# Performance work log

Measured on AMD Instinct MI355X. Metric: run time of the kernel, lower is better.

The kernel has to match this reference:

```python
import jax, jax.numpy as jnp
import numpy as np
from jax import lax


def _layernorm(x, g, b, eps=1e-5):
    m = x.mean(-1, keepdims=True)
    v = ((x - m) ** 2).mean(-1, keepdims=True)
    return (x - m) * lax.rsqrt(v + eps) * g + b


def _conv1d(x, w, b):
    # x: (B, T, Cin), w: (K, Cin, Cout) -> SAME padding (kernel=3, pad=1)
    y = lax.conv_general_dilated(x, w, (1,), 'SAME',
                                 dimension_numbers=('NWC', 'WIO', 'NWC'))
    return y + b


def _predictor(x, params, mask):
    w1, b1, g1, be1, w2, b2, g2, be2, wl, bl = params
    h = _layernorm(jax.nn.relu(_conv1d(x, w1, b1)), g1, be1)
    h = _layernorm(jax.nn.relu(_conv1d(h, w2, b2)), g2, be2)
    out = (h @ wl)[..., 0] + bl[0]          # (B, T)
    return jnp.where(mask, 0.0, out)


def _length_regulate(x, dur, max_len):
    # vectorized equivalent of the per-token expand/cat/pad loop
    cum = jnp.cumsum(dur, axis=1)            # (B, S)
    mel_len = cum[:, -1]                     # (B,)
    pos = jnp.arange(max_len)                # (T,)
    idx = jax.vmap(lambda c: jnp.searchsorted(c, pos, side='right'))(cum)
    idx = jnp.minimum(idx, x.shape[1] - 1)   # (B, T)
    out = jnp.take_along_axis(x, idx[:, :, None], axis=1)
    valid = (pos[None, :] < mel_len[:, None])[:, :, None]
    return jnp.where(valid, out, 0.0), mel_len


def setup_inputs() -> dict:
    key = jax.random.key(0)
    ks = jax.random.split(key, 12)
    B, S, D, F, K, T, NB = 32, 512, 512, 512, 3, 4096, 256
    inp = {
        'x': jax.random.normal(ks[0], (B, S, D), jnp.float32),
        'src_mask': jnp.zeros((B, S), bool),
        'mel_mask': jnp.zeros((B, T), bool),
        'pitch_truth': jax.random.normal(ks[1], (B, S), jnp.float32),
        'energy_truth': jax.random.normal(ks[2], (B, S), jnp.float32),
        'duration_truth': jax.random.randint(ks[3], (B, S), 0, 8, jnp.int32),
        'conv1_w': 0.05 * jax.random.normal(ks[4], (3, K, D, F), jnp.float32),
        'conv1_b': jnp.zeros((3, F), jnp.float32),
        'ln1_g': jnp.ones((3, F), jnp.float32),
        'ln1_b': jnp.zeros((3, F), jnp.float32),
        'conv2_w': 0.05 * jax.random.normal(ks[5], (3, K, F, F), jnp.float32),
        'conv2_b': jnp.zeros((3, F), jnp.float32),
        'ln2_g': jnp.ones((3, F), jnp.float32),
        'ln2_b': jnp.zeros((3, F), jnp.float32),
        'lin_w': 0.05 * jax.random.normal(ks[6], (3, F, 1), jnp.float32),
        'lin_b': jnp.zeros((3, 1), jnp.float32),
        'pitch_emb': 0.05 * jax.random.normal(ks[7], (NB, D), jnp.float32),
        'energy_emb': 0.05 * jax.random.normal(ks[8], (NB, D), jnp.float32),
        'pitch_bins': jnp.linspace(-3.0, 3.0, NB - 1),
        'energy_bins': jnp.linspace(-3.0, 3.0, NB - 1),
        'max_mel_len': T,
    }
    return inp


def reference(x, src_mask, mel_mask, pitch_truth, energy_truth, duration_truth,
              conv1_w, conv1_b, ln1_g, ln1_b, conv2_w, conv2_b, ln2_g, ln2_b,
              lin_w, lin_b, pitch_emb, energy_emb, pitch_bins, energy_bins,
              max_mel_len):
    def params(i):
        return (conv1_w[i], conv1_b[i], ln1_g[i], ln1_b[i],
                conv2_w[i], conv2_b[i], ln2_g[i], ln2_b[i], lin_w[i], lin_b[i])

    # pitch (predictor idx 0)
    pitch_pred = _predictor(x, params(0), src_mask)
    x = x + pitch_emb[jnp.searchsorted(pitch_bins, pitch_truth, side='left')]
    # energy (idx 1)
    energy_pred = _predictor(x, params(1), src_mask)
    x = x + energy_emb[jnp.searchsorted(energy_bins, energy_truth, side='left')]
    # duration (idx 2)
    log_dur = _predictor(x, params(2), src_mask)
    # length regulation with ground-truth durations (training path)
    x_out, mel_len = _length_regulate(x, duration_truth, max_mel_len)
    return x_out, pitch_pred, energy_pred, log_dur, mel_len, mel_mask
```

## Files before the change

kernel.cpp:

```cpp
#include <hip/hip_runtime.h>
#include <hip/hip_bf16.h>


#define B_ 32
#define S_ 512
#define D_ 512
#define F_ 512
#define T_ 4096
#define SP_ 514
#define KK_ 1536
#define NKT 24

typedef __attribute__((ext_vector_type(8))) short bf16x8;
typedef __attribute__((ext_vector_type(4))) float f32x4;

__device__ __forceinline__ float bf2f(unsigned short u) {
  union { unsigned int i; float f; } c; c.i = (unsigned int)u << 16; return c.f;
}
__device__ __forceinline__ unsigned short f2bf(float f) {
  __hip_bfloat16 h = __float2bfloat16(f);
  return *(unsigned short*)&h;
}

#define WT_BLKS 1152
#define TP_BLKS 8224
__global__ __launch_bounds__(256) void prep_k(const float* __restrict__ x,
                                              const float* __restrict__ W1,
                                              const float* __restrict__ W2,
                                              const int* __restrict__ dur,
                                              __hip_bfloat16* __restrict__ X0,
                                              __hip_bfloat16* __restrict__ X,
                                              __hip_bfloat16* __restrict__ P,
                                              __hip_bfloat16* __restrict__ WT1,
                                              __hip_bfloat16* __restrict__ WT2,
                                              int* __restrict__ cum,
                                              float* __restrict__ mel_len) {
  const int blk = blockIdx.x;
  const int t = threadIdx.x;
  if (blk < WT_BLKS) {
    __shared__ float tb[64][65];
    const int w = blk / 192;
    const int kt = (blk % 192) >> 3;
    const int ft = blk & 7;
    const float* src = (w < 3) ? (W1 + (size_t)w * KK_ * F_)
                               : (W2 + (size_t)(w - 3) * KK_ * F_);
    __hip_bfloat16* dst = (w < 3) ? (WT1 + (size_t)w * KK_ * F_)
                                  : (WT2 + (size_t)(w - 3) * KK_ * F_);
    const int ty = t >> 4, tx = t & 15;
    #pragma unroll
    for (int j = 0; j < 4; ++j) {
      const int r = ty + j * 16;
      const float4 v = *(const float4*)(src + (size_t)(kt * 64 + r) * F_ + ft * 64 + tx * 4);
      tb[r][tx * 4 + 0] = v.x; tb[r][tx * 4 + 1] = v.y;
      tb[r][tx * 4 + 2] = v.z; tb[r][tx * 4 + 3] = v.w;
    }
    __syncthreads();
    #pragma unroll
    for (int j = 0; j < 4; ++j) {
      const int r = ty + j * 16;
      ushort4 u = make_ushort4(f2bf(tb[tx * 4 + 0][r]), f2bf(tb[tx * 4 + 1][r]),
                               f2bf(tb[tx * 4 + 2][r]), f2bf(tb[tx * 4 + 3][r]));
      *(ushort4*)((unsigned short*)dst + (size_t)(ft * 64 + r) * KK_ + kt * 64 + tx * 4) = u;
    }
  } else if (blk < WT_BLKS + TP_BLKS) {
    const int task = (blk - WT_BLKS) * 2 + (t >> 7);
    const int tl = t & 127;
    if (task < B_ * S_) {
      const int b = task >> 9, s = task & 511;
      const float4 v = *(const float4*)(x + (size_t)task * D_ + tl * 4);
      ushort4 u = make_ushort4(f2bf(v.x), f2bf(v.y), f2bf(v.z), f2bf(v.w));
      *(ushort4*)((unsigned short*)X0 + ((size_t)b * SP_ + s + 1) * D_ + tl * 4) = u;
    } else {
      const int idx = task - B_ * S_;
      const int b = idx >> 1;
      const int r = (idx & 1) ? (SP_ - 1) : 0;
      const size_t off = ((size_t)b * SP_ + r) * D_ + tl * 4;
      const ushort4 z = make_ushort4(0, 0, 0, 0);
      *(ushort4*)((unsigned short*)X0 + off) = z;
      *(ushort4*)((unsigned short*)X + off) = z;
      *(ushort4*)((unsigned short*)P + off) = z;
    }
  } else {
    __shared__ int sh[S_];
    const int b = blk - (WT_BLKS + TP_BLKS);
    sh[t] = dur[b * S_ + t];
    sh[t + 256] = dur[b * S_ + t + 256];
    __syncthreads();
    for (int off = 1; off < S_; off <<= 1) {
      const int a1 = (t >= off) ? sh[t - off] : 0;
      const int j2 = t + 256;
      const int a2 = (j2 >= off) ? sh[j2 - off] : 0;
      __syncthreads();
      sh[t] += a1; sh[j2] += a2;
      __syncthreads();
    }
    cum[b * S_ + t] = sh[t];
    cum[b * S_ + t + 256] = sh[t + 256];
    if (t == 255) mel_len[b] = (float)sh[S_ - 1];
  }
}

template <int MODE>
__global__ __launch_bounds__(512, 1) void convfuse_k(
    const __hip_bfloat16* __restrict__ Pin,
    const __hip_bfloat16* __restrict__ WT,
    const float* __restrict__ bias,
    const float* __restrict__ g,
    const float* __restrict__ be,
    const float* __restrict__ wl,
    const float* __restrict__ bl,
    const unsigned char* __restrict__ mask,
    __hip_bfloat16* __restrict__ Pout,
    float* __restrict__ pred,
    const float* __restrict__ truth,
    const float* __restrict__ bins,
    const float* __restrict__ embp,
    const __hip_bfloat16* __restrict__ Xsrc,
    __hip_bfloat16* __restrict__ Xdst) {
  extern __shared__ char smem[];
  char* As = smem;
  char* Bs = smem + 2 * 8192;
  const int swz = (blockIdx.x & 7) * 32 + (blockIdx.x >> 3);
  const int b  = swz >> 3;
  const int st = (swz & 7) * 64;
  const int t = threadIdx.x;
  const int lane = t & 63;
  const int wave = t >> 6;
  const int wn = wave * 64;

  f32x4 acc[4][4];
  #pragma unroll
  for (int m = 0; m < 4; ++m)
    #pragma unroll
    for (int n = 0; n < 4; ++n) acc[m][n] = (f32x4){0.f, 0.f, 0.f, 0.f};

  const __hip_bfloat16* Xb = Pin + (size_t)b * SP_ * D_;

  auto stage = [&](int kt, int buf) {
    const int tap = kt >> 3, d0 = (kt & 7) * 64;
    const __hip_bfloat16* Arow = Xb + (size_t)(st + tap) * D_ + d0;
    char* Ad = As + buf * 8192;
    {
      const int row = t >> 3, ch = t & 7;
      const __hip_bfloat16* ga = Arow + (size_t)row * D_ + (ch ^ (row & 7)) * 8;
      __builtin_amdgcn_global_load_lds(
          (const __attribute__((address_space(1))) void*)ga,
          (__attribute__((address_space(3))) void*)(Ad + t * 16), 16, 0, 0);
    }
    char* Bd = Bs + buf * 65536;
    #pragma unroll
    for (int i = 0; i < 8; ++i) {
      const int c = t + i * 512;
      const int fr = c >> 3, ch = c & 7;
      const __hip_bfloat16* gb = WT + (size_t)fr * KK_ + kt * 64 + (ch ^ (fr & 7)) * 8;
      __builtin_amdgcn_global_load_lds(
          (const __attribute__((address_space(1))) void*)gb,
          (__attribute__((address_space(3))) void*)(Bd + c * 16), 16, 0, 0);
    }
  };

  stage(0, 0);
  const int rA = lane & 15;
  const int kc16 = (lane >> 4) * 16;
  const int sw = (rA & 7) << 4;

  for (int kt = 0; kt < NKT; ++kt) {
    const int cur = kt & 1;
    if (kt < NKT - 1) {
      stage(kt + 1, cur ^ 1);
      asm volatile("s_waitcnt vmcnt(9)" ::: "memory");
    } else {
      asm volatile("s_waitcnt vmcnt(0)" ::: "memory");
    }
    __builtin_amdgcn_s_barrier();
    __builtin_amdgcn_sched_barrier(0);
    const char* Ab = As + cur * 8192;
    const char* Bb = Bs + cur * 65536;
    #pragma unroll
    for (int kh = 0; kh < 2; ++kh) {
      const int offx = (kh * 64 + kc16) ^ sw;
      bf16x8 af[4], bf[4];
      #pragma unroll
      for (int m = 0; m < 4; ++m)
        af[m] = *(const bf16x8*)(Ab + (m * 16 + rA) * 128 + offx);
      #pragma unroll
      for (int n = 0; n < 4; ++n)
        bf[n] = *(const bf16x8*)(Bb + (wn + n * 16 + rA) * 128 + offx);
      __builtin_amdgcn_s_setprio(1);
      #pragma unroll
      for (int m = 0; m < 4; ++m)
        #pragma unroll
        for (int n = 0; n < 4; ++n)
          acc[m][n] = __builtin_amdgcn_mfma_f32_16x16x32_bf16(af[m], bf[n], acc[m][n], 0, 0, 0);
      __builtin_amdgcn_s_setprio(0);
    }
    __builtin_amdgcn_sched_barrier(0);
    __builtin_amdgcn_s_barrier();
  }

  float* rS = (float*)smem;
  float* rQ = rS + 512;
  float* rP = rQ + 512;
  float* tS = rP + 512;
  float* tQ = tS + 64;
  float* tP = tQ + 64;
  float* wG = tP + 64;
  float* wB = wG + 8;

  float bia[4], gg[4], bb[4], ww[4];
  #pragma unroll
  for (int n = 0; n < 4; ++n) {
    const int f = wn + n * 16 + rA;
    bia[n] = bias[f]; gg[n] = g[f]; bb[n] = be[f];
    if (MODE == 1) ww[n] = wl[f];
  }
  if (MODE == 1) {
    float gwp = 0.f, bwp = 0.f;
    #pragma unroll
    for (int n = 0; n < 4; ++n) { gwp += gg[n] * ww[n]; bwp += bb[n] * ww[n]; }
    #pragma unroll
    for (int o = 1; o < 16; o <<= 1) {
      gwp += __shfl_xor(gwp, o); bwp += __shfl_xor(bwp, o);
    }
    if (lane == 0) { wG[wave] = gwp; wB[wave] = bwp; }
  }
  #pragma unroll
  for (int m = 0; m < 4; ++m) {
    #pragma unroll
    for (int r = 0; r < 4; ++r) {
      float sv = 0.f, sq = 0.f, sp = 0.f;
      #pragma unroll
      for (int n = 0; n < 4; ++n) {
        float v = fmaxf(acc[m][n][r] + bia[n], 0.f);
        acc[m][n][r] = v;
        sv += v; sq += v * v;
        if (MODE == 1) sp += v * gg[n] * ww[n];
      }
      #pragma unroll
      for (int o = 1; o < 16; o <<= 1) {
        sv += __shfl_xor(sv, o); sq += __shfl_xor(sq, o);
        if (MODE == 1) sp += __shfl_xor(sp, o);
      }
      if (rA == 0) {
        const int row = m * 16 + (lane >> 4) * 4 + r;
        rS[wave * 64 + row] = sv; rQ[wave * 64 + row] = sq;
        if (MODE == 1) rP[wave * 64 + row] = sp;
      }
    }
  }
  __syncthreads();
  if (t < 64) {
    float S = 0.f, Q = 0.f, Pp = 0.f;
    #pragma unroll
    for (int w = 0; w < 8; ++w) {
      S += rS[w * 64 + t]; Q += rQ[w * 64 + t];
      if (MODE == 1) Pp += rP[w * 64 + t];
    }
    tS[t] = S; tQ[t] = Q;
    if (MODE == 1) tP[t] = Pp;
  }
  __syncthreads();
  if (MODE == 0) {
    unsigned short* Pu = (unsigned short*)Pout;
    #pragma unroll
    for (int m = 0; m < 4; ++m) {
      #pragma unroll
      for (int r = 0; r < 4; ++r) {
        const int row = m * 16 + (lane >> 4) * 4 + r;
        const float mean = tS[row] * (1.f / F_);
        const float var = tQ[row] * (1.f / F_) - mean * mean;
        const float inv = rsqrtf(var + 1e-5f);
        unsigned short* pp =
            Pu + ((size_t)b * SP_ + st + row + 1) * D_ + wn + rA;
        #pragma unroll
        for (int n = 0; n < 4; ++n)
          pp[n * 16] = f2bf((acc[m][n][r] - mean) * inv * gg[n] + bb[n]);
      }
    }
  } else {
    if (t < 64) {
      float GW = 0.f, BW = 0.f;
      #pragma unroll
      for (int w = 0; w < 8; ++w) { GW += wG[w]; BW += wB[w]; }
      const float mean = tS[t] * (1.f / F_);
      const float var = tQ[t] * (1.f / F_) - mean * mean;
      const float inv = rsqrtf(var + 1e-5f);
      const int grow = b * S_ + st + t;
      pred[grow] = mask[grow] ? 0.f
                              : (inv * tP[t] - inv * mean * GW + BW + bl[0]);
    }
    if (truth != nullptr) {
      __syncthreads();
      int* aidx = (int*)(smem + 8192);
      if (t < 64) {
        const float v = truth[b * S_ + st + t];
        int lo = 0, hi = 255;
        while (lo < hi) { const int mid = (lo + hi) >> 1; if (bins[mid] < v) lo = mid + 1; else hi = mid; }
        aidx[t] = lo;
      }
      __syncthreads();
      const int sub = t >> 7;
      const int tl = t & 127;
      #pragma unroll
      for (int it = 0; it < 16; ++it) {
        const int r = it * 4 + sub;
        const int e = aidx[r];
        const size_t off = ((size_t)b * SP_ + st + r + 1) * D_ + tl * 4;
        const ushort4 ui = *(const ushort4*)((const unsigned short*)Xsrc + off);
        const float4 ev = *(const float4*)(embp + (size_t)e * D_ + tl * 4);
        ushort4 u = make_ushort4(f2bf(bf2f(ui.x) + ev.x), f2bf(bf2f(ui.y) + ev.y),
                                 f2bf(bf2f(ui.z) + ev.z), f2bf(bf2f(ui.w) + ev.w));
        *(ushort4*)((unsigned short*)Xdst + off) = u;
      }
    }
  }
}

__global__ __launch_bounds__(256) void gather_k(const __hip_bfloat16* __restrict__ X,
                                                const int* __restrict__ cum,
                                                const unsigned char* __restrict__ melm,
                                                float* __restrict__ out,
                                                float* __restrict__ maskf) {
  const int b    = blockIdx.x >> 11;
  const int pos0 = (blockIdx.x & 2047) * 2;
  const int half = threadIdx.x >> 7;
  const int tl   = threadIdx.x & 127;
  const int pos  = pos0 + half;
  __shared__ int sidx[2], svalid[2];
  if (tl == 0) {
    const int* c = cum + b * S_;
    int lo = 0, hi = S_;
    while (lo < hi) {
      const int mid = (lo + hi) >> 1;
      if (c[mid] <= pos) lo = mid + 1; else hi = mid;
    }
    sidx[half] = (lo < S_ - 1) ? lo : (S_ - 1);
    svalid[half] = (pos < c[S_ - 1]) ? 1 : 0;
    maskf[(size_t)b * T_ + pos] = melm[(size_t)b * T_ + pos] ? 1.f : 0.f;
  }
  __syncthreads();
  float4 v = make_float4(0.f, 0.f, 0.f, 0.f);
  if (svalid[half]) {
    const ushort4 u = *(const ushort4*)((const unsigned short*)X +
                        ((size_t)b * SP_ + sidx[half] + 1) * D_ + tl * 4);
    v = make_float4(bf2f(u.x), bf2f(u.y), bf2f(u.z), bf2f(u.w));
  }
  *(float4*)(out + ((size_t)b * T_ + pos) * D_ + tl * 4) = v;
}

extern "C" void kernel_launch(void* const* d_in, const int* in_sizes, int n_in,
                              void* d_out, int out_size, void* d_ws, size_t ws_size,
                              hipStream_t stream) {
  const float* x            = (const float*)d_in[0];
  const unsigned char* srcm = (const unsigned char*)d_in[1];
  const unsigned char* melm = (const unsigned char*)d_in[2];
  const float* pitch_truth  = (const float*)d_in[3];
  const float* energy_truth = (const float*)d_in[4];
  const int*   dur          = (const int*)d_in[5];
  const float* conv1_w = (const float*)d_in[6];
  const float* conv1_b = (const float*)d_in[7];
  const float* ln1_g   = (const float*)d_in[8];
  const float* ln1_b   = (const float*)d_in[9];
  const float* conv2_w = (const float*)d_in[10];
  const float* conv2_b = (const float*)d_in[11];
  const float* ln2_g   = (const float*)d_in[12];
  const float* ln2_b   = (const float*)d_in[13];
  const float* lin_w   = (const float*)d_in[14];
  const float* lin_b   = (const float*)d_in[15];
  const float* pitch_emb   = (const float*)d_in[16];
  const float* energy_emb  = (const float*)d_in[17];
  const float* pitch_bins  = (const float*)d_in[18];
  const float* energy_bins = (const float*)d_in[19];

  float* out      = (float*)d_out;
  float* x_out    = out;
  float* p_pitch  = out + (size_t)B_ * T_ * D_;
  float* p_energy = p_pitch + B_ * S_;
  float* p_dur    = p_energy + B_ * S_;
  float* p_mellen = p_dur + B_ * S_;
  float* p_mask   = p_mellen + B_;

  __hip_bfloat16* X0  = (__hip_bfloat16*)d_ws;
  __hip_bfloat16* X   = X0 + (size_t)B_ * SP_ * D_;
  __hip_bfloat16* P   = X + (size_t)B_ * SP_ * D_;
  __hip_bfloat16* WT1 = P + (size_t)B_ * SP_ * D_;
  __hip_bfloat16* WT2 = WT1 + (size_t)3 * F_ * KK_;
  int*  cum = (int*)(WT2 + (size_t)3 * F_ * KK_);

  const dim3 blk512t(512), blk256(256);
  const dim3 convGrid(256);

  const int convLds = 2 * (8192 + 65536);
  hipFuncSetAttribute((const void*)convfuse_k<0>,
                      hipFuncAttributeMaxDynamicSharedMemorySize, convLds);
  hipFuncSetAttribute((const void*)convfuse_k<1>,
                      hipFuncAttributeMaxDynamicSharedMemorySize, convLds);

  prep_k<<<dim3(WT_BLKS + TP_BLKS + B_), blk256, 0, stream>>>(
      x, conv1_w, conv2_w, dur, X0, X, P, WT1, WT2, cum, p_mellen);

  auto predictor = [&](const __hip_bfloat16* in, int i, float* pred,
                       const float* truth, const float* bins, const float* emb,
                       const __hip_bfloat16* Xsrc, __hip_bfloat16* Xdst) {
    convfuse_k<0><<<convGrid, blk512t, convLds, stream>>>(
        in, WT1 + (size_t)i * F_ * KK_, conv1_b + (size_t)i * F_,
        ln1_g + (size_t)i * F_, ln1_b + (size_t)i * F_,
        nullptr, nullptr, nullptr, P, nullptr,
        nullptr, nullptr, nullptr, nullptr, nullptr);
    convfuse_k<1><<<convGrid, blk512t, convLds, stream>>>(
        P, WT2 + (size_t)i * F_ * KK_, conv2_b + (size_t)i * F_,
        ln2_g + (size_t)i * F_, ln2_b + (size_t)i * F_,
        lin_w + (size_t)i * F_, lin_b + i, srcm, nullptr, pred,
        truth, bins, emb, Xsrc, Xdst);
  };

  predictor(X0, 0, p_pitch, pitch_truth, pitch_bins, pitch_emb, X0, X);
  predictor(X, 1, p_energy, energy_truth, energy_bins, energy_emb, X, X);
  predictor(X, 2, p_dur, nullptr, nullptr, nullptr, nullptr, nullptr);

  gather_k<<<dim3(B_ * T_ / 2), blk256, 0, stream>>>(X, cum, melm, x_out, p_mask);
}
```

Before: 369.7 us.

## Precompute embedding-shifted inputs and batch independent predictor convs into grouped launches

```diff
diff --git a/kernel.cpp b/kernel.cpp
--- a/kernel.cpp
+++ b/kernel.cpp
@@ -9,7 +9,8 @@
 #define T_ 4096
 #define SP_ 514
 #define KK_ 1536
-#define NKT 24
+#define NKT 48
+#define SLOT ((size_t)B_ * SP_ * D_)
 
 typedef __attribute__((ext_vector_type(8))) short bf16x8;
 typedef __attribute__((ext_vector_type(4))) float f32x4;
@@ -21,6 +22,20 @@
   __hip_bfloat16 h = __float2bfloat16(f);
   return *(unsigned short*)&h;
 }
+
+struct Job {
+  const __hip_bfloat16* Pin;
+  const __hip_bfloat16* WT;
+  const float* bias;
+  const float* g;
+  const float* be;
+  const float* wl;
+  const float* bl;
+  const unsigned char* mask;
+  __hip_bfloat16* Pout;
+  float* pred;
+  int mode;
+};
 
 #define WT_BLKS 1152
 #define TP_BLKS 8224
@@ -28,9 +43,17 @@
                                               const float* __restrict__ W1,
                                               const float* __restrict__ W2,
                                               const int* __restrict__ dur,
+                                              const float* __restrict__ ptruth,
+                                              const float* __restrict__ pbins,
+                                              const float* __restrict__ pemb,
+                                              const float* __restrict__ etruth,
+                                              const float* __restrict__ ebins,
+                                              const float* __restrict__ eemb,
                                               __hip_bfloat16* __restrict__ X0,
-                                              __hip_bfloat16* __restrict__ X,
-                                              __hip_bfloat16* __restrict__ P,
+                                              __hip_bfloat16* __restrict__ X1,
+                                              __hip_bfloat16* __restrict__ X2,
+                                              __hip_bfloat16* __restrict__ P0,
+                                              __hip_bfloat16* __restrict__ P1,
                                               __hip_bfloat16* __restrict__ WT1,
                                               __hip_bfloat16* __restrict__ WT2,
                                               int* __restrict__ cum,
@@ -63,22 +86,46 @@
       *(ushort4*)((unsigned short*)dst + (size_t)(ft * 64 + r) * KK_ + kt * 64 + tx * 4) = u;
     }
   } else if (blk < WT_BLKS + TP_BLKS) {
-    const int task = (blk - WT_BLKS) * 2 + (t >> 7);
+    __shared__ int i1s[2], i2s[2];
+    const int half = t >> 7;
     const int tl = t & 127;
+    const int task = (blk - WT_BLKS) * 2 + half;
     if (task < B_ * S_) {
+      if (tl == 0) {
+        float v = ptruth[task];
+        int lo = 0, hi = 255;
+        while (lo < hi) { const int mid = (lo + hi) >> 1; if (pbins[mid] < v) lo = mid + 1; else hi = mid; }
+        i1s[half] = lo;
+        v = etruth[task]; lo = 0; hi = 255;
+        while (lo < hi) { const int mid = (lo + hi) >> 1; if (ebins[mid] < v) lo = mid + 1; else hi = mid; }
+        i2s[half] = lo;
+      }
+      __syncthreads();
       const int b = task >> 9, s = task & 511;
+      const size_t off = ((size_t)b * SP_ + s + 1) * D_ + tl * 4;
       const float4 v = *(const float4*)(x + (size_t)task * D_ + tl * 4);
-      ushort4 u = make_ushort4(f2bf(v.x), f2bf(v.y), f2bf(v.z), f2bf(v.w));
-      *(ushort4*)((unsigned short*)X0 + ((size_t)b * SP_ + s + 1) * D_ + tl * 4) = u;
+      const float4 pe = *(const float4*)(pemb + (size_t)i1s[half] * D_ + tl * 4);
+      const float4 ee = *(const float4*)(eemb + (size_t)i2s[half] * D_ + tl * 4);
+      *(ushort4*)((unsigned short*)X0 + off) =
+          make_ushort4(f2bf(v.x), f2bf(v.y), f2bf(v.z), f2bf(v.w));
+      const float4 v1 = make_float4(v.x + pe.x, v.y + pe.y, v.z + pe.z, v.w + pe.w);
+      *(ushort4*)((unsigned short*)X1 + off) =
+          make_ushort4(f2bf(v1.x), f2bf(v1.y), f2bf(v1.z), f2bf(v1.w));
+      *(ushort4*)((unsigned short*)X2 + off) =
+          make_ushort4(f2bf(v1.x + ee.x), f2bf(v1.y + ee.y),
+                       f2bf(v1.z + ee.z), f2bf(v1.w + ee.w));
     } else {
+      __syncthreads();
       const int idx = task - B_ * S_;
       const int b = idx >> 1;
       const int r = (idx & 1) ? (SP_ - 1) : 0;
       const size_t off = ((size_t)b * SP_ + r) * D_ + tl * 4;
       const ushort4 z = make_ushort4(0, 0, 0, 0);
       *(ushort4*)((unsigned short*)X0 + off) = z;
-      *(ushort4*)((unsigned short*)X + off) = z;
-      *(ushort4*)((unsigned short*)P + off) = z;
+      *(ushort4*)((unsigned short*)X1 + off) = z;
+      *(ushort4*)((unsigned short*)X2 + off) = z;
+      *(ushort4*)((unsigned short*)P0 + off) = z;
+      *(ushort4*)((unsigned short*)P1 + off) = z;
     }
   } else {
     __shared__ int sh[S_];
@@ -100,27 +147,14 @@
   }
 }
 
-template <int MODE>
-__global__ __launch_bounds__(512, 1) void convfuse_k(
-    const __hip_bfloat16* __restrict__ Pin,
-    const __hip_bfloat16* __restrict__ WT,
-    const float* __restrict__ bias,
-    const float* __restrict__ g,
-    const float* __restrict__ be,
-    const float* __restrict__ wl,
-    const float* __restrict__ bl,
-    const unsigned char* __restrict__ mask,
-    __hip_bfloat16* __restrict__ Pout,
-    float* __restrict__ pred,
-    const float* __restrict__ truth,
-    const float* __restrict__ bins,
-    const float* __restrict__ embp,
-    const __hip_bfloat16* __restrict__ Xsrc,
-    __hip_bfloat16* __restrict__ Xdst) {
+__global__ __launch_bounds__(512, 4) void convfuse_k(Job j0, Job j1, Job j2) {
   extern __shared__ char smem[];
   char* As = smem;
-  char* Bs = smem + 2 * 8192;
-  const int swz = (blockIdx.x & 7) * 32 + (blockIdx.x >> 3);
+  char* Bs = smem + 2 * 4096;
+  const int pid = blockIdx.x >> 8;
+  const Job jb = (pid == 0) ? j0 : (pid == 1 ? j1 : j2);
+  const int inner = blockIdx.x & 255;
+  const int swz = (inner & 7) * 32 + (inner >> 3);
   const int b  = swz >> 3;
   const int st = (swz & 7) * 64;
   const int t = threadIdx.x;
@@ -134,25 +168,26 @@
     #pragma unroll
     for (int n = 0; n < 4; ++n) acc[m][n] = (f32x4){0.f, 0.f, 0.f, 0.f};
 
-  const __hip_bfloat16* Xb = Pin + (size_t)b * SP_ * D_;
+  const __hip_bfloat16* Xb = jb.Pin + (size_t)b * SP_ * D_;
+  const __hip_bfloat16* WT = jb.WT;
 
   auto stage = [&](int kt, int buf) {
-    const int tap = kt >> 3, d0 = (kt & 7) * 64;
-    const __hip_bfloat16* Arow = Xb + (size_t)(st + tap) * D_ + d0;
-    char* Ad = As + buf * 8192;
-    {
-      const int row = t >> 3, ch = t & 7;
-      const __hip_bfloat16* ga = Arow + (size_t)row * D_ + (ch ^ (row & 7)) * 8;
+    char* Ad = As + buf * 4096;
+    if (t < 256) {
+      const int row = t >> 2, ch = t & 3;
+      const __hip_bfloat16* ga = Xb + (size_t)(st + (kt >> 4) + row) * D_ +
+                                 (kt & 15) * 32 + (ch ^ ((row >> 1) & 3)) * 8;
       __builtin_amdgcn_global_load_lds(
           (const __attribute__((address_space(1))) void*)ga,
           (__attribute__((address_space(3))) void*)(Ad + t * 16), 16, 0, 0);
     }
-    char* Bd = Bs + buf * 65536;
-    #pragma unroll
-    for (int i = 0; i < 8; ++i) {
+    char* Bd = Bs + buf * 32768;
+    #pragma unroll
+    for (int i = 0; i < 4; ++i) {
       const int c = t + i * 512;
-      const int fr = c >> 3, ch = c & 7;
-      const __hip_bfloat16* gb = WT + (size_t)fr * KK_ + kt * 64 + (ch ^ (fr & 7)) * 8;
+      const int fr = c >> 2, ch = c & 3;
+      const __hip_bfloat16* gb = WT + (size_t)fr * KK_ + kt * 32 +
+                                 (ch ^ ((fr >> 1) & 3)) * 8;
       __builtin_amdgcn_global_load_lds(
           (const __attribute__((address_space(1))) void*)gb,
           (__attribute__((address_space(3))) void*)(Bd + c * 16), 16, 0, 0);
@@ -160,42 +195,30 @@
   };
 
   stage(0, 0);
+  __syncthreads();
   const int rA = lane & 15;
-  const int kc16 = (lane >> 4) * 16;
-  const int sw = (rA & 7) << 4;
+  const int offx = ((lane >> 4) * 16) ^ (((rA >> 1) & 3) << 4);
 
   for (int kt = 0; kt < NKT; ++kt) {
     const int cur = kt & 1;
-    if (kt < NKT - 1) {
-      stage(kt + 1, cur ^ 1);
-      asm volatile("s_waitcnt vmcnt(9)" ::: "memory");
-    } else {
-      asm volatile("s_waitcnt vmcnt(0)" ::: "memory");
-    }
-    __builtin_amdgcn_s_barrier();
-    __builtin_amdgcn_sched_barrier(0);
-    const char* Ab = As + cur * 8192;
-    const char* Bb = Bs + cur * 65536;
-    #pragma unroll
-    for (int kh = 0; kh < 2; ++kh) {
-      const int offx = (kh * 64 + kc16) ^ sw;
-      bf16x8 af[4], bf[4];
-      #pragma unroll
-      for (int m = 0; m < 4; ++m)
-        af[m] = *(const bf16x8*)(Ab + (m * 16 + rA) * 128 + offx);
+    if (kt < NKT - 1) stage(kt + 1, cur ^ 1);
+    const char* Ab = As + cur * 4096;
+    const char* Bb = Bs + cur * 32768;
+    bf16x8 af[4], bf[4];
+    #pragma unroll
+    for (int m = 0; m < 4; ++m)
+      af[m] = *(const bf16x8*)(Ab + (m * 16 + rA) * 64 + offx);
+    #pragma unroll
+    for (int n = 0; n < 4; ++n)
+      bf[n] = *(const bf16x8*)(Bb + (wn + n * 16 + rA) * 64 + offx);
+    __builtin_amdgcn_s_setprio(1);
+    #pragma unroll
+    for (int m = 0; m < 4; ++m)
       #pragma unroll
       for (int n = 0; n < 4; ++n)
-        bf[n] = *(const bf16x8*)(Bb + (wn + n * 16 + rA) * 128 + offx);
-      __builtin_amdgcn_s_setprio(1);
-      #pragma unroll
-      for (int m = 0; m < 4; ++m)
-        #pragma unroll
-        for (int n = 0; n < 4; ++n)
-          acc[m][n] = __builtin_amdgcn_mfma_f32_16x16x32_bf16(af[m], bf[n], acc[m][n], 0, 0, 0);
-      __builtin_amdgcn_s_setprio(0);
-    }
-    __builtin_amdgcn_sched_barrier(0);
-    __builtin_amdgcn_s_barrier();
+        acc[m][n] = __builtin_amdgcn_mfma_f32_16x16x32_bf16(af[m], bf[n], acc[m][n], 0, 0, 0);
+    __builtin_amdgcn_s_setprio(0);
+    __syncthreads();
   }
 
   float* rS = (float*)smem;
@@ -207,12 +230,13 @@
   float* wG = tP + 64;
   float* wB = wG + 8;
 
+  const int MODE = jb.mode;
   float bia[4], gg[4], bb[4], ww[4];
   #pragma unroll
   for (int n = 0; n < 4; ++n) {
     const int f = wn + n * 16 + rA;
-    bia[n] = bias[f]; gg[n] = g[f]; bb[n] = be[f];
-    if (MODE == 1) ww[n] = wl[f];
+    bia[n] = jb.bias[f]; gg[n] = jb.g[f]; bb[n] = jb.be[f];
+    ww[n] = (MODE == 1) ? jb.wl[f] : 0.f;
   }
   if (MODE == 1) {
     float gwp = 0.f, bwp = 0.f;
@@ -234,17 +258,17 @@
         float v = fmaxf(acc[m][n][r] + bia[n], 0.f);
         acc[m][n][r] = v;
         sv += v; sq += v * v;
-        if (MODE == 1) sp += v * gg[n] * ww[n];
+        sp += v * gg[n] * ww[n];
       }
       #pragma unroll
       for (int o = 1; o < 16; o <<= 1) {
         sv += __shfl_xor(sv, o); sq += __shfl_xor(sq, o);
-        if (MODE == 1) sp += __shfl_xor(sp, o);
+        sp += __shfl_xor(sp, o);
       }
       if (rA == 0) {
         const int row = m * 16 + (lane >> 4) * 4 + r;
         rS[wave * 64 + row] = sv; rQ[wave * 64 + row] = sq;
-        if (MODE == 1) rP[wave * 64 + row] = sp;
+        rP[wave * 64 + row] = sp;
       }
     }
   }
@@ -253,15 +277,13 @@
     float S = 0.f, Q = 0.f, Pp = 0.f;
     #pragma unroll
     for (int w = 0; w < 8; ++w) {
-      S += rS[w * 64 + t]; Q += rQ[w * 64 + t];
-      if (MODE == 1) Pp += rP[w * 64 + t];
-    }
-    tS[t] = S; tQ[t] = Q;
-    if (MODE == 1) tP[t] = Pp;
+      S += rS[w * 64 + t]; Q += rQ[w * 64 + t]; Pp += rP[w * 64 + t];
+    }
+    tS[t] = S; tQ[t] = Q; tP[t] = Pp;
   }
   __syncthreads();
   if (MODE == 0) {
-    unsigned short* Pu = (unsigned short*)Pout;
+    unsigned short* Pu = (unsigned short*)jb.Pout;
     #pragma unroll
     for (int m = 0; m < 4; ++m) {
       #pragma unroll
@@ -286,32 +308,8 @@
       const float var = tQ[t] * (1.f / F_) - mean * mean;
       const float inv = rsqrtf(var + 1e-5f);
       const int grow = b * S_ + st + t;
-      pred[grow] = mask[grow] ? 0.f
-                              : (inv * tP[t] - inv * mean * GW + BW + bl[0]);
-    }
-    if (truth != nullptr) {
-      __syncthreads();
-      int* aidx = (int*)(smem + 8192);
-      if (t < 64) {
-        const float v = truth[b * S_ + st + t];
-        int lo = 0, hi = 255;
-        while (lo < hi) { const int mid = (lo + hi) >> 1; if (bins[mid] < v) lo = mid + 1; else hi = mid; }
-        aidx[t] = lo;
-      }
-      __syncthreads();
-      const int sub = t >> 7;
-      const int tl = t & 127;
-      #pragma unroll
-      for (int it = 0; it < 16; ++it) {
-        const int r = it * 4 + sub;
-        const int e = aidx[r];
-        const size_t off = ((size_t)b * SP_ + st + r + 1) * D_ + tl * 4;
-        const ushort4 ui = *(const ushort4*)((const unsigned short*)Xsrc + off);
-        const float4 ev = *(const float4*)(embp + (size_t)e * D_ + tl * 4);
-        ushort4 u = make_ushort4(f2bf(bf2f(ui.x) + ev.x), f2bf(bf2f(ui.y) + ev.y),
-                                 f2bf(bf2f(ui.z) + ev.z), f2bf(bf2f(ui.w) + ev.w));
-        *(ushort4*)((unsigned short*)Xdst + off) = u;
-      }
+      jb.pred[grow] = jb.mask[grow] ? 0.f
+                                    : (inv * tP[t] - inv * mean * GW + BW + jb.bl[0]);
     }
   }
 }
@@ -380,43 +378,48 @@
   float* p_mellen = p_dur + B_ * S_;
   float* p_mask   = p_mellen + B_;
 
-  __hip_bfloat16* X0  = (__hip_bfloat16*)d_ws;
-  __hip_bfloat16* X   = X0 + (size_t)B_ * SP_ * D_;
-  __hip_bfloat16* P   = X + (size_t)B_ * SP_ * D_;
-  __hip_bfloat16* WT1 = P + (size_t)B_ * SP_ * D_;
+  __hip_bfloat16* S0  = (__hip_bfloat16*)d_ws;
+  __hip_bfloat16* S1  = S0 + SLOT;
+  __hip_bfloat16* S2  = S1 + SLOT;
+  __hip_bfloat16* S3  = S2 + SLOT;
+  __hip_bfloat16* S4  = S3 + SLOT;
+  __hip_bfloat16* WT1 = S4 + SLOT;
   __hip_bfloat16* WT2 = WT1 + (size_t)3 * F_ * KK_;
   int*  cum = (int*)(WT2 + (size_t)3 * F_ * KK_);
 
   const dim3 blk512t(512), blk256(256);
-  const dim3 convGrid(256);
-
-  const int convLds = 2 * (8192 + 65536);
-  hipFuncSetAttribute((const void*)convfuse_k<0>,
+  const int convLds = 2 * (4096 + 32768);
+  hipFuncSetAttribute((const void*)convfuse_k,
                       hipFuncAttributeMaxDynamicSharedMemorySize, convLds);
-  hipFuncSetAttribute((const void*)convfuse_k<1>,
-                      hipFuncAttributeMaxDynamicSharedMemorySize, convLds);
 
   prep_k<<<dim3(WT_BLKS + TP_BLKS + B_), blk256, 0, stream>>>(
-      x, conv1_w, conv2_w, dur, X0, X, P, WT1, WT2, cum, p_mellen);
-
-  auto predictor = [&](const __hip_bfloat16* in, int i, float* pred,
-                       const float* truth, const float* bins, const float* emb,
-                       const __hip_bfloat16* Xsrc, __hip_bfloat16* Xdst) {
-    convfuse_k<0><<<convGrid, blk512t, convLds, stream>>>(
-        in, WT1 + (size_t)i * F_ * KK_, conv1_b + (size_t)i * F_,
-        ln1_g + (size_t)i * F_, ln1_b + (size_t)i * F_,
-        nullptr, nullptr, nullptr, P, nullptr,
-        nullptr, nullptr, nullptr, nullptr, nullptr);
-    convfuse_k<1><<<convGrid, blk512t, convLds, stream>>>(
-        P, WT2 + (size_t)i * F_ * KK_, conv2_b + (size_t)i * F_,
-        ln2_g + (size_t)i * F_, ln2_b + (size_t)i * F_,
-        lin_w + (size_t)i * F_, lin_b + i, srcm, nullptr, pred,
-        truth, bins, emb, Xsrc, Xdst);
+      x, conv1_w, conv2_w, dur, pitch_truth, pitch_bins, pitch_emb,
+      energy_truth, energy_bins, energy_emb,
+      S0, S1, S2, S3, S4, WT1, WT2, cum, p_mellen);
+
+  auto c1 = [&](int i, const __hip_bfloat16* in, __hip_bfloat16* Pout) {
+    return Job{in, WT1 + (size_t)i * F_ * KK_, conv1_b + (size_t)i * F_,
+               ln1_g + (size_t)i * F_, ln1_b + (size_t)i * F_,
+               nullptr, nullptr, nullptr, Pout, nullptr, 0};
   };
-
-  predictor(X0, 0, p_pitch, pitch_truth, pitch_bins, pitch_emb, X0, X);
-  predictor(X, 1, p_energy, energy_truth, energy_bins, energy_emb, X, X);
-  predictor(X, 2, p_dur, nullptr, nullptr, nullptr, nullptr, nullptr);
-
-  gather_k<<<dim3(B_ * T_ / 2), blk256, 0, stream>>>(X, cum, melm, x_out, p_mask);
-}
+  auto c2 = [&](int i, const __hip_bfloat16* in, float* pred) {
+    return Job{in, WT2 + (size_t)i * F_ * KK_, conv2_b + (size_t)i * F_,
+               ln2_g + (size_t)i * F_, ln2_b + (size_t)i * F_,
+               lin_w + (size_t)i * F_, lin_b + i, srcm, nullptr, pred, 1};
+  };
+
+  {
+    Job a = c1(0, S0, S3), b = c1(1, S1, S4);
+    convfuse_k<<<dim3(512), blk512t, convLds, stream>>>(a, b, b);
+  }
+  {
+    Job a = c2(0, S3, p_pitch), b = c2(1, S4, p_energy), c = c1(2, S2, S0);
+    convfuse_k<<<dim3(768), blk512t, convLds, stream>>>(a, b, c);
+  }
+  {
+    Job a = c2(2, S0, p_dur);
+    convfuse_k<<<dim3(256), blk512t, convLds, stream>>>(a, a, a);
+  }
+
+  gather_k<<<dim3(B_ * T_ / 2), blk256, 0, stream>>>(S2, cum, melm, x_out, p_mask);
+}
```

New measurement: 379.3 us. +2.6%, slower.
